# Kernel tuning notes

Hardware: AMD Instinct MI355X
Metric: run time of the kernel (lower is better)

The kernel has to match this reference:

```python
import jax, jax.numpy as jnp
import numpy as np

IN_C, OUT_C, K, STRIDE, PAD = 64, 128, 3, 1, 1


def setup_inputs() -> dict:
    key = jax.random.key(0)
    kx, kw = jax.random.split(key)
    x = jax.random.normal(kx, (16, IN_C, 112, 112), dtype=jnp.float32)
    scale = np.sqrt(2.0 / (IN_C * K * K)).astype(np.float32)
    weight = jax.random.normal(kw, (OUT_C, IN_C, K, K), dtype=jnp.float32) * scale
    bias = jnp.zeros((OUT_C,), dtype=jnp.float32)
    return {"x": x, "weight": weight, "bias": bias}


def reference(x, weight, bias):
    # Direct 2D convolution (cross-correlation, like torch Conv2d), NCHW layout.
    out = jax.lax.conv_general_dilated(
        x, weight,
        window_strides=(STRIDE, STRIDE),
        padding=((PAD, PAD), (PAD, PAD)),
        dimension_numbers=("NCHW", "OIHW", "NCHW"),
    )
    return out + bias[None, :, None, None]
```

## Files before the change

kernel.cpp:

```cpp
#include <hip/hip_runtime.h>
#include <stdint.h>


#define HW      112
#define PIX     12544
#define ICN     64
#define OCN     128
#define PADW    114
#define PADPIX  12996
#define NIMG    16

#define XT_BYTES  (NIMG * PADPIX * ICN * 2)
#define WT_OFF    XT_BYTES
#define XPB       204
#define XBLK      (NIMG * XPB)
#define WBLK      72
#define CONV_BLK  (NIMG * 56)

typedef __attribute__((ext_vector_type(8))) __bf16 bf16x8;
typedef __attribute__((ext_vector_type(4))) float  f32x4;

__device__ __forceinline__ uint32_t rne_lo(float f) {
    uint32_t u = __builtin_bit_cast(uint32_t, f);
    return (u + 0x7fffu + ((u >> 16) & 1u)) >> 16;
}
__device__ __forceinline__ uint32_t pk2(float a, float b) {
    uint32_t ub = __builtin_bit_cast(uint32_t, b);
    ub = (ub + 0x7fffu + ((ub >> 16) & 1u)) & 0xffff0000u;
    return rne_lo(a) | ub;
}
__device__ __forceinline__ void load_lds16(const void* g, void* l) {
    __builtin_amdgcn_global_load_lds(
        (const __attribute__((address_space(1))) uint32_t*)g,
        (__attribute__((address_space(3))) uint32_t*)l, 16, 0, 0);
}

__global__ void __launch_bounds__(256)
prep(const float* __restrict__ x, const float* __restrict__ w, uint8_t* __restrict__ ws) {
    const int b = blockIdx.x;
    const int t = threadIdx.x;

    if (b < XBLK) {
        const int n  = b / XPB;
        const int pp = (b - n * XPB) * 64 + (t >> 2);
        const int q  = t & 3;
        if (pp >= PADPIX) return;
        char* dst = (char*)ws + ((size_t)(n * PADPIX + pp)) * 128 + q * 32;
        const int hp = pp / PADW;
        const int wp = pp - hp * PADW;
        if (hp >= 1 && hp <= HW && wp >= 1 && wp <= HW) {
            const int p = (hp - 1) * HW + (wp - 1);
            const float* src = x + ((size_t)n * ICN + q * 16) * PIX + p;
            float v[16];
#pragma unroll
            for (int i = 0; i < 16; ++i) v[i] = src[(size_t)i * PIX];
            *(uint4*)dst        = make_uint4(pk2(v[0], v[1]),   pk2(v[2], v[3]),
                                             pk2(v[4], v[5]),   pk2(v[6], v[7]));
            *(uint4*)(dst + 16) = make_uint4(pk2(v[8], v[9]),   pk2(v[10], v[11]),
                                             pk2(v[12], v[13]), pk2(v[14], v[15]));
        } else {
            *(uint4*)dst        = make_uint4(0, 0, 0, 0);
            *(uint4*)(dst + 16) = make_uint4(0, 0, 0, 0);
        }
    } else {
        uint16_t* wt = (uint16_t*)(ws + WT_OFF);
        const int wb = b - XBLK;
#pragma unroll
        for (int k = 0; k < 4; ++k) {
            int wi = wb * 1024 + k * 256 + t;
            int r  = wi >> 13;
            int oc = (wi >> 6) & 127;
            int ic = wi & 63;
            wt[wi] = (uint16_t)rne_lo(w[oc * 576 + ic * 9 + r]);
        }
    }
}

__global__ void __launch_bounds__(256, 2)
conv_mfma(const uint8_t* __restrict__ ws, const float* __restrict__ bias,
          float* __restrict__ out) {
    __shared__ uint8_t Xs[4 * PADW * 128];

    const char* xt = (const char*)ws;
    const char* wt = (const char*)(ws + WT_OFF);

    const int t = threadIdx.x;
    const int b = blockIdx.x;
    const int n  = b / 56;
    const int tr = b - n * 56;
    const int h0 = tr * 2;

    const int lane = t & 63;
    const int wave = t >> 6;
    const int lr = lane & 15;
    const int lq = lane >> 4;
    const int oc_base = (wave & 1) * 64;
    const int pxb = wave >> 1;

    {
        const char* hbase = xt + ((size_t)(n * PADPIX + h0 * PADW)) * 128;
#pragma unroll
        for (int i = 0; i < 14; ++i) {
            const int idx = i * 256 + t;
            const int r = idx >> 3, c = idx & 7;
            load_lds16(hbase + r * 128 + ((c ^ (r & 7)) * 16),
                       (char*)Xs + (i * 256 + wave * 64) * 16);
        }
        if (wave == 0) {
            const int idx = 14 * 256 + t;
            const int r = idx >> 3, c = idx & 7;
            load_lds16(hbase + r * 128 + ((c ^ (r & 7)) * 16),
                       (char*)Xs + (14 * 256) * 16);
        }
    }
    __syncthreads();

    f32x4 acc[4][7];
    {
        f32x4 z = {0.f, 0.f, 0.f, 0.f};
#pragma unroll
        for (int i = 0; i < 4; ++i)
#pragma unroll
            for (int j = 0; j < 7; ++j) acc[i][j] = z;
    }

    const char* abase = wt + (oc_base + lr) * 128 + lq * 16;

#pragma unroll
    for (int tap = 0; tap < 9; ++tap) {
        const int dy = tap / 3 - 1;
        const int dx = tap - (tap / 3) * 3 - 1;
        const int rb = (pxb + dy + 1) * PADW + dx + 1 + lr;
        const int s0 = ((lq)     ^ (rb & 7)) * 16;
        const int s1 = ((lq + 4) ^ (rb & 7)) * 16;
        const char* bbase = (const char*)Xs + rb * 128;

        bf16x8 a[8];
#pragma unroll
        for (int mi = 0; mi < 4; ++mi) {
            a[mi * 2]     = *(const bf16x8*)(abase + tap * 16384 + mi * 2048);
            a[mi * 2 + 1] = *(const bf16x8*)(abase + tap * 16384 + mi * 2048 + 64);
        }
#pragma unroll
        for (int ni = 0; ni < 7; ++ni) {
            bf16x8 b0 = *(const bf16x8*)(bbase + ni * 2048 + s0);
            bf16x8 b1 = *(const bf16x8*)(bbase + ni * 2048 + s1);
#pragma unroll
            for (int mi = 0; mi < 4; ++mi) {
                acc[mi][ni] = __builtin_amdgcn_mfma_f32_16x16x32_bf16(
                    a[mi * 2],     b0, acc[mi][ni], 0, 0, 0);
                acc[mi][ni] = __builtin_amdgcn_mfma_f32_16x16x32_bf16(
                    a[mi * 2 + 1], b1, acc[mi][ni], 0, 0, 0);
            }
        }
    }

    const int oh = h0 + pxb;
#pragma unroll
    for (int mi = 0; mi < 4; ++mi) {
#pragma unroll
        for (int rg = 0; rg < 4; ++rg) {
            const int oc = oc_base + mi * 16 + lq * 4 + rg;
            const float bb = bias[oc];
            float* orow = out + ((size_t)(n * OCN + oc)) * PIX + oh * HW + lr;
#pragma unroll
            for (int ni = 0; ni < 7; ++ni)
                orow[ni * 16] = acc[mi][ni][rg] + bb;
        }
    }
}

extern "C" void kernel_launch(void* const* d_in, const int* in_sizes, int n_in,
                              void* d_out, int out_size, void* d_ws, size_t ws_size,
                              hipStream_t stream) {
    const float* x    = (const float*)d_in[0];
    const float* w    = (const float*)d_in[1];
    const float* bias = (const float*)d_in[2];
    float* out = (float*)d_out;
    uint8_t* ws = (uint8_t*)d_ws;

    prep<<<XBLK + WBLK, 256, 0, stream>>>(x, w, ws);
    conv_mfma<<<CONV_BLK, 256, 0, stream>>>(ws, bias, out);
}
```

Baseline: 187.6 us.

## Coalesce NCHW-to-NHWC prep via LDS transpose and tile conv by single output row

The prep kernel now reads 256 contiguous pixels per block across all 64 channels with coalesced loads. It transposes them through padded shared memory and writes 16-byte NHWC bf16 chunks. A separate set of blocks zeroes only the padding border. The conv kernel now gives each block one output row with four waves each owning 32 output channels, which cuts LDS to three input rows and allows three blocks per CU. The trade is more blocks that each reload the input halo rows, plus separate weight fragment loads per wave.

```diff
diff --git a/kernel.cpp b/kernel.cpp
--- a/kernel.cpp
+++ b/kernel.cpp
@@ -12,10 +12,11 @@
 
 #define XT_BYTES  (NIMG * PADPIX * ICN * 2)
 #define WT_OFF    XT_BYTES
-#define XPB       204
-#define XBLK      (NIMG * XPB)
+#define PXB       49
+#define XBLK      (NIMG * PXB)
+#define ZBLK      226
 #define WBLK      72
-#define CONV_BLK  (NIMG * 56)
+#define CONV_BLK  (NIMG * HW)
 
 typedef __attribute__((ext_vector_type(8))) __bf16 bf16x8;
 typedef __attribute__((ext_vector_type(4))) float  f32x4;
@@ -37,34 +38,50 @@
 
 __global__ void __launch_bounds__(256)
 prep(const float* __restrict__ x, const float* __restrict__ w, uint8_t* __restrict__ ws) {
+    __shared__ uint32_t S[256 * 33];
     const int b = blockIdx.x;
     const int t = threadIdx.x;
 
     if (b < XBLK) {
-        const int n  = b / XPB;
-        const int pp = (b - n * XPB) * 64 + (t >> 2);
-        const int q  = t & 3;
-        if (pp >= PADPIX) return;
-        char* dst = (char*)ws + ((size_t)(n * PADPIX + pp)) * 128 + q * 32;
-        const int hp = pp / PADW;
-        const int wp = pp - hp * PADW;
-        if (hp >= 1 && hp <= HW && wp >= 1 && wp <= HW) {
-            const int p = (hp - 1) * HW + (wp - 1);
-            const float* src = x + ((size_t)n * ICN + q * 16) * PIX + p;
-            float v[16];
+        const int n  = b / PXB;
+        const int p0 = (b - n * PXB) * 256;
+        const float* src = x + (size_t)n * ICN * PIX + p0 + t;
 #pragma unroll
-            for (int i = 0; i < 16; ++i) v[i] = src[(size_t)i * PIX];
-            *(uint4*)dst        = make_uint4(pk2(v[0], v[1]),   pk2(v[2], v[3]),
-                                             pk2(v[4], v[5]),   pk2(v[6], v[7]));
-            *(uint4*)(dst + 16) = make_uint4(pk2(v[8], v[9]),   pk2(v[10], v[11]),
-                                             pk2(v[12], v[13]), pk2(v[14], v[15]));
-        } else {
-            *(uint4*)dst        = make_uint4(0, 0, 0, 0);
-            *(uint4*)(dst + 16) = make_uint4(0, 0, 0, 0);
+        for (int j = 0; j < 32; ++j) {
+            float f0 = src[(size_t)(2 * j) * PIX];
+            float f1 = src[(size_t)(2 * j + 1) * PIX];
+            S[t * 33 + j] = pk2(f0, f1);
         }
+        __syncthreads();
+#pragma unroll
+        for (int wv = 0; wv < 8; ++wv) {
+            const int c   = wv * 256 + t;
+            const int pxl = c >> 3;
+            const int icc = c & 7;
+            const uint32_t* sp = &S[pxl * 33 + icc * 4];
+            uint4 v = make_uint4(sp[0], sp[1], sp[2], sp[3]);
+            const int px = p0 + pxl;
+            const int h  = px / HW;
+            const int wd = px - h * HW;
+            char* dst = (char*)ws +
+                ((size_t)(n * PADPIX + (h + 1) * PADW + wd + 1)) * 128 + icc * 16;
+            *(uint4*)dst = v;
+        }
+    } else if (b < XBLK + ZBLK) {
+        const int g    = (b - XBLK) * 256 + t;
+        const int img  = g / 3616;
+        const int rem  = g - img * 3616;
+        const int pxi  = rem >> 3;
+        const int icc  = rem & 7;
+        int hp, wp;
+        if (pxi < PADW)            { hp = 0;   wp = pxi; }
+        else if (pxi < 2 * PADW)   { hp = 113; wp = pxi - PADW; }
+        else { int j = pxi - 2 * PADW; hp = 1 + (j >> 1); wp = (j & 1) * 113; }
+        char* dst = (char*)ws + ((size_t)(img * PADPIX + hp * PADW + wp)) * 128 + icc * 16;
+        *(uint4*)dst = make_uint4(0, 0, 0, 0);
     } else {
         uint16_t* wt = (uint16_t*)(ws + WT_OFF);
-        const int wb = b - XBLK;
+        const int wb = b - XBLK - ZBLK;
 #pragma unroll
         for (int k = 0; k < 4; ++k) {
             int wi = wb * 1024 + k * 256 + t;
@@ -76,91 +93,82 @@
     }
 }
 
-__global__ void __launch_bounds__(256, 2)
+__global__ void __launch_bounds__(256, 3)
 conv_mfma(const uint8_t* __restrict__ ws, const float* __restrict__ bias,
           float* __restrict__ out) {
-    __shared__ uint8_t Xs[4 * PADW * 128];
+    __shared__ uint8_t Xs[3 * PADW * 128];
 
     const char* xt = (const char*)ws;
     const char* wt = (const char*)(ws + WT_OFF);
 
     const int t = threadIdx.x;
     const int b = blockIdx.x;
-    const int n  = b / 56;
-    const int tr = b - n * 56;
-    const int h0 = tr * 2;
+    const int n  = b / HW;
+    const int oh = b - n * HW;
 
     const int lane = t & 63;
     const int wave = t >> 6;
     const int lr = lane & 15;
     const int lq = lane >> 4;
-    const int oc_base = (wave & 1) * 64;
-    const int pxb = wave >> 1;
+    const int oc_w = wave * 32;
 
     {
-        const char* hbase = xt + ((size_t)(n * PADPIX + h0 * PADW)) * 128;
+        const char* hbase = xt + ((size_t)(n * PADPIX + oh * PADW)) * 128;
 #pragma unroll
-        for (int i = 0; i < 14; ++i) {
+        for (int i = 0; i < 10; ++i) {
             const int idx = i * 256 + t;
             const int r = idx >> 3, c = idx & 7;
-            load_lds16(hbase + r * 128 + ((c ^ (r & 7)) * 16),
-                       (char*)Xs + (i * 256 + wave * 64) * 16);
+            load_lds16(hbase + r * 128 + ((c ^ (r & 7)) * 16), (char*)Xs + idx * 16);
         }
-        if (wave == 0) {
-            const int idx = 14 * 256 + t;
+        if (t < 176) {
+            const int idx = 2560 + t;
             const int r = idx >> 3, c = idx & 7;
-            load_lds16(hbase + r * 128 + ((c ^ (r & 7)) * 16),
-                       (char*)Xs + (14 * 256) * 16);
+            load_lds16(hbase + r * 128 + ((c ^ (r & 7)) * 16), (char*)Xs + idx * 16);
         }
     }
     __syncthreads();
 
-    f32x4 acc[4][7];
+    f32x4 acc[2][7];
     {
         f32x4 z = {0.f, 0.f, 0.f, 0.f};
 #pragma unroll
-        for (int i = 0; i < 4; ++i)
+        for (int i = 0; i < 2; ++i)
 #pragma unroll
             for (int j = 0; j < 7; ++j) acc[i][j] = z;
     }
 
-    const char* abase = wt + (oc_base + lr) * 128 + lq * 16;
+    const char* abase = wt + (oc_w + lr) * 128 + lq * 16;
 
 #pragma unroll
     for (int tap = 0; tap < 9; ++tap) {
         const int dy = tap / 3 - 1;
         const int dx = tap - (tap / 3) * 3 - 1;
-        const int rb = (pxb + dy + 1) * PADW + dx + 1 + lr;
-        const int s0 = ((lq)     ^ (rb & 7)) * 16;
-        const int s1 = ((lq + 4) ^ (rb & 7)) * 16;
-        const char* bbase = (const char*)Xs + rb * 128;
+        const int r0 = (dy + 1) * PADW + dx + 1 + lr;
+        const int r7 = r0 & 7;
+        const int s0 = (lq ^ r7) * 16;
+        const int s1 = s0 ^ 64;
+        const char* bbase = (const char*)Xs + r0 * 128;
 
-        bf16x8 a[8];
-#pragma unroll
-        for (int mi = 0; mi < 4; ++mi) {
-            a[mi * 2]     = *(const bf16x8*)(abase + tap * 16384 + mi * 2048);
-            a[mi * 2 + 1] = *(const bf16x8*)(abase + tap * 16384 + mi * 2048 + 64);
-        }
+        bf16x8 a0 = *(const bf16x8*)(abase + tap * 16384);
+        bf16x8 a1 = *(const bf16x8*)(abase + tap * 16384 + 64);
+        bf16x8 a2 = *(const bf16x8*)(abase + tap * 16384 + 2048);
+        bf16x8 a3 = *(const bf16x8*)(abase + tap * 16384 + 2048 + 64);
 #pragma unroll
         for (int ni = 0; ni < 7; ++ni) {
             bf16x8 b0 = *(const bf16x8*)(bbase + ni * 2048 + s0);
             bf16x8 b1 = *(const bf16x8*)(bbase + ni * 2048 + s1);
-#pragma unroll
-            for (int mi = 0; mi < 4; ++mi) {
-                acc[mi][ni] = __builtin_amdgcn_mfma_f32_16x16x32_bf16(
-                    a[mi * 2],     b0, acc[mi][ni], 0, 0, 0);
-                acc[mi][ni] = __builtin_amdgcn_mfma_f32_16x16x32_bf16(
-                    a[mi * 2 + 1], b1, acc[mi][ni], 0, 0, 0);
-            }
+            acc[0][ni] = __builtin_amdgcn_mfma_f32_16x16x32_bf16(a0, b0, acc[0][ni], 0, 0, 0);
+            acc[1][ni] = __builtin_amdgcn_mfma_f32_16x16x32_bf16(a2, b0, acc[1][ni], 0, 0, 0);
+            acc[0][ni] = __builtin_amdgcn_mfma_f32_16x16x32_bf16(a1, b1, acc[0][ni], 0, 0, 0);
+            acc[1][ni] = __builtin_amdgcn_mfma_f32_16x16x32_bf16(a3, b1, acc[1][ni], 0, 0, 0);
         }
     }
 
-    const int oh = h0 + pxb;
 #pragma unroll
-    for (int mi = 0; mi < 4; ++mi) {
+    for (int mi = 0; mi < 2; ++mi) {
 #pragma unroll
         for (int rg = 0; rg < 4; ++rg) {
-            const int oc = oc_base + mi * 16 + lq * 4 + rg;
+            const int oc = oc_w + mi * 16 + lq * 4 + rg;
             const float bb = bias[oc];
             float* orow = out + ((size_t)(n * OCN + oc)) * PIX + oh * HW + lr;
 #pragma unroll
@@ -179,6 +187,6 @@
     float* out = (float*)d_out;
     uint8_t* ws = (uint8_t*)d_ws;
 
-    prep<<<XBLK + WBLK, 256, 0, stream>>>(x, w, ws);
+    prep<<<XBLK + ZBLK + WBLK, 256, 0, stream>>>(x, w, ws);
     conv_mfma<<<CONV_BLK, 256, 0, stream>>>(ws, bias, out);
 }
```

Measured after the change: 190.3 us. About the same (+1.4%).
